# Performance work log

Measured on AMD Instinct MI355X. Metric: run time of the kernel, lower is better.

## Reference

```python
import jax, jax.numpy as jnp
import numpy as np
import math

B, S, D = 2, 2048, 2048
H, KVH, WIN = 16, 4, 256
HD = D // H            # 128
QPER = H // KVH        # 4


def setup_inputs() -> dict:
    key = jax.random.key(0)
    ks = jax.random.split(key, 9)
    s = lambda k, shp: jax.random.normal(k, shp, dtype=jnp.float32) * 0.02
    return {
        "x": jax.random.normal(ks[0], (B, S, D), dtype=jnp.float32),
        "Wq": s(ks[1], (D, D)),            "bq": jnp.zeros((D,), jnp.float32),
        "Wk": s(ks[2], (D, KVH * HD)),      "bk": jnp.zeros((KVH * HD,), jnp.float32),
        "Wv": s(ks[3], (D, KVH * HD)),      "bv": jnp.zeros((KVH * HD,), jnp.float32),
        "Wo": s(ks[4], (D, D)),            "bo": jnp.zeros((D,), jnp.float32),
    }


def reference(x, Wq, bq, Wk, bk, Wv, bv, Wo, bo):
    b, s, _ = x.shape
    # projections
    Q = (x @ Wq + bq).reshape(b, s, H, HD).transpose(0, 2, 1, 3)     # [b,H,s,hd]
    K = (x @ Wk + bk).reshape(b, s, KVH, HD).transpose(0, 2, 1, 3)   # [b,kvh,s,hd]
    V = (x @ Wv + bv).reshape(b, s, KVH, HD).transpose(0, 2, 1, 3)   # [b,kvh,s,hd]
    # GQA grouping: head h = g*QPER + q
    Qg = Q.reshape(b, KVH, QPER, s, HD)                               # [b,g,q,s,hd]
    scores = jnp.einsum('bgqsd,bgtd->bgqst', Qg, K)                   # [b,g,q,s,s]
    i = jnp.arange(s)[:, None]
    j = jnp.arange(s)[None, :]
    keep = (j <= i) & (j >= i - WIN + 1)                              # [s,s]
    scores = jnp.where(keep, scores, -jnp.inf)
    A = jax.nn.softmax(scores / math.sqrt(HD), axis=-1)
    O = jnp.einsum('bgqst,bgtd->bgqsd', A, V)                         # [b,g,q,s,hd]
    O = O.reshape(b, H, s, HD).transpose(0, 2, 1, 3).reshape(b, s, D)
    return O @ Wo + bo
```

## Files before the change

### kernel.cpp

```cpp
#include <hip/hip_runtime.h>
#include <hip/hip_bf16.h>
#include <math.h>

typedef __bf16 bf16_t;
typedef bf16_t bf16x8 __attribute__((ext_vector_type(8)));
typedef bf16_t bf16x4 __attribute__((ext_vector_type(4)));
typedef float  f32x4  __attribute__((ext_vector_type(4)));

#define NB    2
#define SEQ   2048
#define DIM   2048
#define NHEAD 16
#define NKVH  4
#define HDIM  128
#define WINSZ 256
#define KVD   512
#define QKVN  3072
#define MROWS 4096

__device__ __forceinline__ void async_copy16(const void* g, void* lds) {
    __builtin_amdgcn_global_load_lds(
        (const __attribute__((address_space(1))) void*)g,
        (__attribute__((address_space(3))) void*)lds,
        16, 0, 0);
}

__global__ __launch_bounds__(256) void cvt_f32_bf16(const float* __restrict__ in,
                                                    bf16_t* __restrict__ out, int n) {
    int i = (blockIdx.x * 256 + threadIdx.x) * 4;
    if (i >= n) return;
    float4 v = *(const float4*)(in + i);
    bf16x4 o;
    o[0] = (bf16_t)v.x; o[1] = (bf16_t)v.y; o[2] = (bf16_t)v.z; o[3] = (bf16_t)v.w;
    *(bf16x4*)(out + i) = o;
}

__global__ __launch_bounds__(256) void transpose_cvt(const float* __restrict__ in,
                                                     bf16_t* __restrict__ out, int K, int N) {
    __shared__ float tile[32][33];
    int tx = threadIdx.x & 31, ty = threadIdx.x >> 5;
    int n0 = blockIdx.x * 32, k0 = blockIdx.y * 32;
    for (int r = ty; r < 32; r += 8)
        tile[r][tx] = in[(size_t)(k0 + r) * N + n0 + tx];
    __syncthreads();
    for (int r = ty; r < 32; r += 8)
        out[(size_t)(n0 + r) * K + k0 + tx] = (bf16_t)tile[tx][r];
}

__global__ __launch_bounds__(256) void concat_bias(const float* __restrict__ bq,
                                                   const float* __restrict__ bk,
                                                   const float* __restrict__ bv,
                                                   float* __restrict__ out) {
    int i = blockIdx.x * 256 + threadIdx.x;
    if (i >= QKVN) return;
    float v = (i < DIM) ? bq[i] : ((i < DIM + KVD) ? bk[i - DIM] : bv[i - DIM - KVD]);
    out[i] = v;
}

__global__ __launch_bounds__(256) void transpose_v(const bf16_t* __restrict__ QKV,
                                                   bf16_t* __restrict__ Vtb) {
    __shared__ bf16_t t[32][33];
    int tx = threadIdx.x & 31, ty = threadIdx.x >> 5;
    int jb = blockIdx.x, c0 = blockIdx.y * 32, b = blockIdx.z;
    int j0 = jb * 32;
    for (int r = ty; r < 32; r += 8)
        t[r][tx] = QKV[((size_t)(b * SEQ) + j0 + r) * QKVN + (DIM + KVD) + c0 + tx];
    __syncthreads();
    int g = c0 >> 7, dl = c0 & 127;
    bf16_t* outb = Vtb + (((size_t)(b * NKVH) + g) * 64 + jb) * 4096;
    for (int r = ty; r < 32; r += 8)
        outb[(dl + r) * 32 + tx] = t[tx][r];
}

template <int BM, int BN, typename OutT>
__global__ __launch_bounds__(512, 1) void gemm8p(const bf16_t* __restrict__ A,
                                                 const bf16_t* __restrict__ Bt,
                                                 const float* __restrict__ bias,
                                                 OutT* __restrict__ C,
                                                 int M, int N, int K, float qs, int qcols) {
    constexpr int ASLOTS = BM / 16;
    constexpr int BSLOTS = BN / 16;
    constexpr int MF   = BM / 32;
    constexpr int NF   = BN / 64;
    constexpr int AHALF = BM * 32;
    constexpr int BHALF = BN * 32;
    constexpr int BUFSZ = 2 * (AHALF + BHALF);
    __shared__ bf16_t lds[2 * BUFSZ];

    const int tid  = threadIdx.x;
    const int wave = tid >> 6;
    const int lane = tid & 63;
    const int lg = lane >> 4, lc = lane & 15;
    const int wr = wave >> 2, wc = wave & 3;

    const int nbn  = N / BN;
    const int nblk = (M / BM) * nbn;
    const int qq   = nblk >> 3;
    const int swz  = (blockIdx.x & 7) * qq + (blockIdx.x >> 3);
    const long brow = (long)(swz / nbn) * BM;
    const long bcol = (long)(swz % nbn) * BN;

    const int aiss = (ASLOTS - wave + 7) >> 3;
    const int biss = (BSLOTS - wave + 7) >> 3;
    const int miss = aiss + biss;

    f32x4 acc[MF][NF] = {};

    auto stage = [&](int buf, int p, int kt) {
        const int kcol = kt * 64 + p * 32;
        const int srow = lane >> 2;
        const int sch  = lane & 3;
        {
            bf16_t* d = lds + buf * BUFSZ + p * AHALF;
#pragma unroll
            for (int s = wave; s < ASLOTS; s += 8) {
                int row = s * 16 + srow;
                int ch  = sch ^ ((row >> 1) & 3);
                async_copy16(A + (brow + row) * (long)K + kcol + ch * 8, d + s * 512);
            }
        }
        {
            bf16_t* d = lds + buf * BUFSZ + 2 * AHALF + p * BHALF;
#pragma unroll
            for (int s = wave; s < BSLOTS; s += 8) {
                int row = s * 16 + srow;
                int ch  = sch ^ ((row >> 1) & 3);
                async_copy16(Bt + (bcol + row) * (long)K + kcol + ch * 8, d + s * 512);
            }
        }
    };

    stage(0, 0, 0);
    stage(0, 1, 0);

    const int NT = K >> 6;
    const int cswz = (lg ^ ((lc >> 1) & 3)) * 8;
    for (int t = 0; t < NT; ++t) {
#pragma unroll
        for (int p = 0; p < 2; ++p) {
            if (t == NT - 1 && p == 1) {
                asm volatile("s_waitcnt vmcnt(0)" ::: "memory");
            } else if (miss == 4) {
                asm volatile("s_waitcnt vmcnt(4)" ::: "memory");
            } else if (miss == 3) {
                asm volatile("s_waitcnt vmcnt(3)" ::: "memory");
            } else {
                asm volatile("s_waitcnt vmcnt(2)" ::: "memory");
            }
            __builtin_amdgcn_s_barrier();
            asm volatile("" ::: "memory");
            const bf16_t* Ab = lds + (t & 1) * BUFSZ + p * AHALF;
            const bf16_t* Bb = lds + (t & 1) * BUFSZ + 2 * AHALF + p * BHALF;
            bf16x8 af[MF], bv[NF];
#pragma unroll
            for (int m = 0; m < MF; ++m)
                af[m] = *(const bf16x8*)(Ab + (wr * (BM / 2) + m * 16 + lc) * 32 + cswz);
#pragma unroll
            for (int n = 0; n < NF; ++n)
                bv[n] = *(const bf16x8*)(Bb + (wc * (BN / 4) + n * 16 + lc) * 32 + cswz);
            if (t + 1 < NT) stage((t + 1) & 1, p, t + 1);
            __builtin_amdgcn_s_setprio(1);
#pragma unroll
            for (int m = 0; m < MF; ++m)
#pragma unroll
                for (int n = 0; n < NF; ++n)
                    acc[m][n] = __builtin_amdgcn_mfma_f32_16x16x32_bf16(af[m], bv[n], acc[m][n], 0, 0, 0);
            __builtin_amdgcn_s_setprio(0);
        }
    }

#pragma unroll
    for (int n = 0; n < NF; ++n) {
        int gc = (int)bcol + wc * (BN / 4) + n * 16 + lc;
        float bvs = bias[gc];
        bool ds = gc < qcols;
#pragma unroll
        for (int m = 0; m < MF; ++m) {
            long gr = brow + wr * (BM / 2) + m * 16 + 4 * lg;
#pragma unroll
            for (int r = 0; r < 4; ++r) {
                float v = acc[m][n][r] + bvs;
                if (ds) v *= qs;
                C[(gr + r) * (long)N + gc] = (OutT)v;
            }
        }
    }
}

__global__ __launch_bounds__(256) void attn_kernel(const bf16_t* __restrict__ QKV,
                                                   const bf16_t* __restrict__ Vtb,
                                                   bf16_t* __restrict__ Ob) {
    __shared__ bf16_t Kls[2][32 * 128];
    __shared__ bf16_t Vls[2][128 * 32];
    __shared__ bf16_t Pls[4][16 * 40];

    const int wv   = threadIdx.x >> 6;
    const int lane = threadIdx.x & 63;
    const int lg = lane >> 4, lc = lane & 15;

    const int swb = (blockIdx.x & 7) * 128 + (blockIdx.x >> 3);
    const int ti = swb & 127;
    const int g  = (swb >> 7) & 3;
    const int b  = swb >> 9;
    const int h  = g * 4 + wv;
    const int i0 = ti * 16;
    const int irow = i0 + lc;
    bf16_t* P = &Pls[wv][0];

    bf16x8 qf[4];
    {
        const bf16_t* qp = QKV + ((size_t)(b * SEQ) + irow) * QKVN + h * HDIM + lg * 8;
#pragma unroll
        for (int kk = 0; kk < 4; ++kk) qf[kk] = *(const bf16x8*)(qp + kk * 32);
    }

    auto stage = [&](int buf, int jb) {
        const int j0s = jb * 32;
        const bf16_t* kgb = QKV + ((size_t)(b * SEQ) + j0s) * QKVN + DIM + g * HDIM;
#pragma unroll
        for (int ii = 0; ii < 2; ++ii) {
            int i = wv * 2 + ii;
            int row = i * 4 + (lane >> 4);
            int ch  = (lane & 15) ^ (row & 7);
            async_copy16(kgb + (size_t)row * QKVN + ch * 8, &Kls[buf][i * 512]);
        }
        const bf16_t* vgb = Vtb + (((size_t)(b * NKVH) + g) * 64 + jb) * 4096;
#pragma unroll
        for (int ii = 0; ii < 2; ++ii) {
            int i = wv * 2 + ii;
            int row = i * 16 + (lane >> 2);
            int ch  = (lane & 3) ^ ((row ^ (row >> 2)) & 3);
            async_copy16(vgb + row * 32 + ch * 8, &Vls[buf][i * 512]);
        }
    };

    float m_run = -1e30f, l_run = 0.f;
    f32x4 oacc[8] = {};

    int jlo = i0 - (WINSZ - 1); if (jlo < 0) jlo = 0;
    const int jb0 = jlo >> 5;
    const int jb1 = (i0 + 15) >> 5;

    stage(0, jb0);

    for (int jb = jb0; jb <= jb1; ++jb) {
        const int j0 = jb * 32;
        const int cur = (jb - jb0) & 1;
        asm volatile("s_waitcnt vmcnt(0)" ::: "memory");
        __builtin_amdgcn_s_barrier();
        asm volatile("" ::: "memory");

        bf16x8 kf[2][4];
#pragma unroll
        for (int t = 0; t < 2; ++t)
#pragma unroll
            for (int kk = 0; kk < 4; ++kk) {
                int row = t * 16 + lc;
                int ch  = (kk * 4 + lg) ^ (row & 7);
                kf[t][kk] = *(const bf16x8*)(&Kls[cur][row * 128 + ch * 8]);
            }
        if (jb < jb1) stage(cur ^ 1, jb + 1);
        asm volatile("s_waitcnt lgkmcnt(0)" ::: "memory");
        __builtin_amdgcn_sched_barrier(0);

        f32x4 s[2];
        __builtin_amdgcn_s_setprio(1);
#pragma unroll
        for (int t = 0; t < 2; ++t) {
            f32x4 sv = {};
#pragma unroll
            for (int kk = 0; kk < 4; ++kk)
                sv = __builtin_amdgcn_mfma_f32_16x16x32_bf16(kf[t][kk], qf[kk], sv, 0, 0, 0);
            s[t] = sv;
        }
        __builtin_amdgcn_s_setprio(0);

        const bool edge = (j0 < i0 - 240) || (j0 > i0 - 31);
        if (edge) {
#pragma unroll
            for (int t = 0; t < 2; ++t)
#pragma unroll
                for (int r = 0; r < 4; ++r) {
                    int j = j0 + t * 16 + 4 * lg + r;
                    if (j > irow || j < irow - (WINSZ - 1)) s[t][r] = -1e30f;
                }
        }
        float tmax = fmaxf(fmaxf(fmaxf(s[0][0], s[0][1]), fmaxf(s[0][2], s[0][3])),
                           fmaxf(fmaxf(s[1][0], s[1][1]), fmaxf(s[1][2], s[1][3])));
        tmax = fmaxf(tmax, __shfl_xor(tmax, 16, 64));
        tmax = fmaxf(tmax, __shfl_xor(tmax, 32, 64));
        if (!__all(tmax - m_run <= 8.0f)) {
            float m_new = fmaxf(m_run, tmax);
            float resc = __builtin_amdgcn_exp2f(m_run - m_new);
            l_run *= resc;
#pragma unroll
            for (int c = 0; c < 8; ++c) {
                oacc[c][0] *= resc; oacc[c][1] *= resc;
                oacc[c][2] *= resc; oacc[c][3] *= resc;
            }
            m_run = m_new;
        }
        float psum = 0.f;
#pragma unroll
        for (int t = 0; t < 2; ++t) {
            bf16x4 pk;
#pragma unroll
            for (int r = 0; r < 4; ++r) {
                float sv = s[t][r];
                float p = (edge && sv < -5e29f) ? 0.f : __builtin_amdgcn_exp2f(sv - m_run);
                psum += p;
                pk[r] = (bf16_t)p;
            }
            *(bf16x4*)(P + lc * 40 + t * 16 + lg * 4) = pk;
        }
        psum += __shfl_xor(psum, 16, 64);
        psum += __shfl_xor(psum, 32, 64);
        l_run += psum;
        asm volatile("" ::: "memory");

        bf16x8 vf[8];
#pragma unroll
        for (int c = 0; c < 8; ++c) {
            int row = c * 16 + lc;
            int ch  = lg ^ ((row ^ (row >> 2)) & 3);
            vf[c] = *(const bf16x8*)(&Vls[cur][row * 32 + ch * 8]);
        }
        bf16x8 pf = *(const bf16x8*)(P + lc * 40 + lg * 8);

        __builtin_amdgcn_s_setprio(1);
#pragma unroll
        for (int c = 0; c < 8; ++c)
            oacc[c] = __builtin_amdgcn_mfma_f32_16x16x32_bf16(vf[c], pf, oacc[c], 0, 0, 0);
        __builtin_amdgcn_s_setprio(0);
    }

    const float inv = 1.f / l_run;
#pragma unroll
    for (int c = 0; c < 8; ++c) {
        bf16x4 ov;
#pragma unroll
        for (int r = 0; r < 4; ++r) ov[r] = (bf16_t)(oacc[c][r] * inv);
        *(bf16x4*)(Ob + ((size_t)(b * SEQ) + irow) * DIM + h * HDIM + c * 16 + lg * 4) = ov;
    }
}

extern "C" void kernel_launch(void* const* d_in, const int* in_sizes, int n_in,
                              void* d_out, int out_size, void* d_ws, size_t ws_size,
                              hipStream_t stream) {
    const float* x  = (const float*)d_in[0];
    const float* Wq = (const float*)d_in[1];
    const float* bq = (const float*)d_in[2];
    const float* Wk = (const float*)d_in[3];
    const float* bk = (const float*)d_in[4];
    const float* Wv = (const float*)d_in[5];
    const float* bv = (const float*)d_in[6];
    const float* Wo = (const float*)d_in[7];
    const float* bo = (const float*)d_in[8];
    float* out = (float*)d_out;

    char* ws = (char*)d_ws;
    bf16_t* xb    = (bf16_t*)(ws);
    bf16_t* WqkvT = (bf16_t*)(ws + (16u << 20));
    bf16_t* WoT   = (bf16_t*)(ws + (28u << 20));
    bf16_t* QKVb  = (bf16_t*)(ws + (36u << 20));
    float*  bqkv  = (float*) (ws + (60u << 20));
    bf16_t* Vtb   = WqkvT;
    bf16_t* Ob    = xb;

    const float qs = 0.12751707498038074f;

    cvt_f32_bf16<<<(MROWS * DIM) / 1024, 256, 0, stream>>>(x, xb, MROWS * DIM);
    transpose_cvt<<<dim3(DIM / 32, DIM / 32), 256, 0, stream>>>(Wq, WqkvT, DIM, DIM);
    transpose_cvt<<<dim3(KVD / 32, DIM / 32), 256, 0, stream>>>(Wk, WqkvT + (size_t)DIM * DIM, DIM, KVD);
    transpose_cvt<<<dim3(KVD / 32, DIM / 32), 256, 0, stream>>>(Wv, WqkvT + (size_t)(DIM + KVD) * DIM, DIM, KVD);
    transpose_cvt<<<dim3(DIM / 32, DIM / 32), 256, 0, stream>>>(Wo, WoT, DIM, DIM);
    concat_bias<<<(QKVN + 255) / 256, 256, 0, stream>>>(bq, bk, bv, bqkv);

    gemm8p<256, 192, bf16_t><<<dim3((MROWS / 256) * (QKVN / 192)), 512, 0, stream>>>(
        xb, WqkvT, bqkv, QKVb, MROWS, QKVN, DIM, qs, DIM);

    transpose_v<<<dim3(SEQ / 32, KVD / 32, NB), 256, 0, stream>>>(QKVb, Vtb);

    attn_kernel<<<dim3(NB * NKVH * (SEQ / 16)), 256, 0, stream>>>(QKVb, Vtb, Ob);

    gemm8p<128, 256, float><<<dim3((MROWS / 128) * (DIM / 256)), 512, 0, stream>>>(
        Ob, WoT, bo, out, MROWS, DIM, DIM, 1.0f, 0);
}
```

Baseline: 160.8 us.

## Process 32 query rows per attention wave and fuse preprocessing kernels

The attention kernel now handles two 16-row query subtiles per wave, so each staged K/V block in LDS feeds twice as many MFMAs. This halves the grid and cuts redundant K/V loads, at the cost of more registers and fewer blocks for occupancy. The six preprocessing launches (x conversion, four weight transposes, bias concat) are merged into one kernel that dispatches on block index, removing per-launch overhead.

Measured after the change: 147.6 us. 1.09x faster.

```diff
diff --git a/kernel.cpp b/kernel.cpp
--- a/kernel.cpp
+++ b/kernel.cpp
@@ -25,36 +25,47 @@
         16, 0, 0);
 }
 
-__global__ __launch_bounds__(256) void cvt_f32_bf16(const float* __restrict__ in,
-                                                    bf16_t* __restrict__ out, int n) {
-    int i = (blockIdx.x * 256 + threadIdx.x) * 4;
-    if (i >= n) return;
-    float4 v = *(const float4*)(in + i);
-    bf16x4 o;
-    o[0] = (bf16_t)v.x; o[1] = (bf16_t)v.y; o[2] = (bf16_t)v.z; o[3] = (bf16_t)v.w;
-    *(bf16x4*)(out + i) = o;
-}
-
-__global__ __launch_bounds__(256) void transpose_cvt(const float* __restrict__ in,
-                                                     bf16_t* __restrict__ out, int K, int N) {
+__global__ __launch_bounds__(256) void preprocess(
+    const float* __restrict__ x,  const float* __restrict__ Wq,
+    const float* __restrict__ bq, const float* __restrict__ Wk,
+    const float* __restrict__ bk, const float* __restrict__ Wv,
+    const float* __restrict__ bv, const float* __restrict__ Wo,
+    bf16_t* __restrict__ xb, bf16_t* __restrict__ WqkvT,
+    bf16_t* __restrict__ WoT, float* __restrict__ bqkv) {
     __shared__ float tile[32][33];
-    int tx = threadIdx.x & 31, ty = threadIdx.x >> 5;
-    int n0 = blockIdx.x * 32, k0 = blockIdx.y * 32;
+    const int tid = threadIdx.x;
+    int bid = blockIdx.x;
+    if (bid < 8192) {
+        int i = (bid * 256 + tid) * 4;
+        float4 v = *(const float4*)(x + i);
+        bf16x4 o;
+        o[0] = (bf16_t)v.x; o[1] = (bf16_t)v.y; o[2] = (bf16_t)v.z; o[3] = (bf16_t)v.w;
+        *(bf16x4*)(xb + i) = o;
+        return;
+    }
+    bid -= 8192;
+    const float* src; bf16_t* dst; int N;
+    if (bid < 4096)       { src = Wq; dst = WqkvT;                          N = DIM; }
+    else if (bid < 5120)  { src = Wk; dst = WqkvT + (size_t)DIM * DIM;      N = KVD; bid -= 4096; }
+    else if (bid < 6144)  { src = Wv; dst = WqkvT + (size_t)(DIM+KVD)*DIM;  N = KVD; bid -= 5120; }
+    else if (bid < 10240) { src = Wo; dst = WoT;                            N = DIM; bid -= 6144; }
+    else {
+        int i = (bid - 10240) * 256 + tid;
+        if (i < QKVN) {
+            float v = (i < DIM) ? bq[i] : ((i < DIM + KVD) ? bk[i - DIM] : bv[i - DIM - KVD]);
+            bqkv[i] = v;
+        }
+        return;
+    }
+    const int K = DIM;
+    int ntile = N / 32;
+    int n0 = (bid % ntile) * 32, k0 = (bid / ntile) * 32;
+    int tx = tid & 31, ty = tid >> 5;
     for (int r = ty; r < 32; r += 8)
-        tile[r][tx] = in[(size_t)(k0 + r) * N + n0 + tx];
+        tile[r][tx] = src[(size_t)(k0 + r) * N + n0 + tx];
     __syncthreads();
     for (int r = ty; r < 32; r += 8)
-        out[(size_t)(n0 + r) * K + k0 + tx] = (bf16_t)tile[tx][r];
-}
-
-__global__ __launch_bounds__(256) void concat_bias(const float* __restrict__ bq,
-                                                   const float* __restrict__ bk,
-                                                   const float* __restrict__ bv,
-                                                   float* __restrict__ out) {
-    int i = blockIdx.x * 256 + threadIdx.x;
-    if (i >= QKVN) return;
-    float v = (i < DIM) ? bq[i] : ((i < DIM + KVD) ? bk[i - DIM] : bv[i - DIM - KVD]);
-    out[i] = v;
+        dst[(size_t)(n0 + r) * K + k0 + tx] = (bf16_t)tile[tx][r];
 }
 
 __global__ __launch_bounds__(256) void transpose_v(const bf16_t* __restrict__ QKV,
@@ -192,26 +203,26 @@
                                                    bf16_t* __restrict__ Ob) {
     __shared__ bf16_t Kls[2][32 * 128];
     __shared__ bf16_t Vls[2][128 * 32];
-    __shared__ bf16_t Pls[4][16 * 40];
+    __shared__ bf16_t Pls[4][32 * 40];
 
     const int wv   = threadIdx.x >> 6;
     const int lane = threadIdx.x & 63;
     const int lg = lane >> 4, lc = lane & 15;
 
-    const int swb = (blockIdx.x & 7) * 128 + (blockIdx.x >> 3);
-    const int ti = swb & 127;
-    const int g  = (swb >> 7) & 3;
-    const int b  = swb >> 9;
+    const int swb = (blockIdx.x & 7) * 64 + (blockIdx.x >> 3);
+    const int ti = swb & 63;
+    const int g  = (swb >> 6) & 3;
+    const int b  = swb >> 8;
     const int h  = g * 4 + wv;
-    const int i0 = ti * 16;
-    const int irow = i0 + lc;
+    const int i0 = ti * 32;
     bf16_t* P = &Pls[wv][0];
 
-    bf16x8 qf[4];
-    {
-        const bf16_t* qp = QKV + ((size_t)(b * SEQ) + irow) * QKVN + h * HDIM + lg * 8;
-#pragma unroll
-        for (int kk = 0; kk < 4; ++kk) qf[kk] = *(const bf16x8*)(qp + kk * 32);
+    bf16x8 qf[2][4];
+#pragma unroll
+    for (int sq = 0; sq < 2; ++sq) {
+        const bf16_t* qp = QKV + ((size_t)(b * SEQ) + i0 + sq * 16 + lc) * QKVN + h * HDIM + lg * 8;
+#pragma unroll
+        for (int kk = 0; kk < 4; ++kk) qf[sq][kk] = *(const bf16x8*)(qp + kk * 32);
     }
 
     auto stage = [&](int buf, int jb) {
@@ -234,12 +245,12 @@
         }
     };
 
-    float m_run = -1e30f, l_run = 0.f;
-    f32x4 oacc[8] = {};
+    float m_run[2] = {-1e30f, -1e30f}, l_run[2] = {0.f, 0.f};
+    f32x4 oacc[2][8] = {};
 
     int jlo = i0 - (WINSZ - 1); if (jlo < 0) jlo = 0;
     const int jb0 = jlo >> 5;
-    const int jb1 = (i0 + 15) >> 5;
+    const int jb1 = (i0 + 31) >> 5;
 
     stage(0, jb0);
 
@@ -263,59 +274,79 @@
         asm volatile("s_waitcnt lgkmcnt(0)" ::: "memory");
         __builtin_amdgcn_sched_barrier(0);
 
-        f32x4 s[2];
+        f32x4 s[2][2];
         __builtin_amdgcn_s_setprio(1);
 #pragma unroll
-        for (int t = 0; t < 2; ++t) {
-            f32x4 sv = {};
-#pragma unroll
-            for (int kk = 0; kk < 4; ++kk)
-                sv = __builtin_amdgcn_mfma_f32_16x16x32_bf16(kf[t][kk], qf[kk], sv, 0, 0, 0);
-            s[t] = sv;
-        }
+        for (int t = 0; t < 2; ++t)
+#pragma unroll
+            for (int sq = 0; sq < 2; ++sq) {
+                f32x4 sv = {};
+#pragma unroll
+                for (int kk = 0; kk < 4; ++kk)
+                    sv = __builtin_amdgcn_mfma_f32_16x16x32_bf16(kf[t][kk], qf[sq][kk], sv, 0, 0, 0);
+                s[t][sq] = sv;
+            }
         __builtin_amdgcn_s_setprio(0);
 
-        const bool edge = (j0 < i0 - 240) || (j0 > i0 - 31);
+        const bool edge = (j0 < i0 - (WINSZ - 32)) || (j0 > i0 - 31);
         if (edge) {
 #pragma unroll
             for (int t = 0; t < 2; ++t)
 #pragma unroll
+                for (int sq = 0; sq < 2; ++sq) {
+                    int irow = i0 + sq * 16 + lc;
+#pragma unroll
+                    for (int r = 0; r < 4; ++r) {
+                        int j = j0 + t * 16 + 4 * lg + r;
+                        if (j > irow || j < irow - (WINSZ - 1)) s[t][sq][r] = -1e30f;
+                    }
+                }
+        }
+        float tmax[2];
+#pragma unroll
+        for (int sq = 0; sq < 2; ++sq) {
+            float tm = fmaxf(fmaxf(fmaxf(s[0][sq][0], s[0][sq][1]), fmaxf(s[0][sq][2], s[0][sq][3])),
+                             fmaxf(fmaxf(s[1][sq][0], s[1][sq][1]), fmaxf(s[1][sq][2], s[1][sq][3])));
+            tm = fmaxf(tm, __shfl_xor(tm, 16, 64));
+            tm = fmaxf(tm, __shfl_xor(tm, 32, 64));
+            tmax[sq] = tm;
+        }
+        if (!__all(tmax[0] - m_run[0] <= 8.0f && tmax[1] - m_run[1] <= 8.0f)) {
+#pragma unroll
+            for (int sq = 0; sq < 2; ++sq) {
+                float m_new = fmaxf(m_run[sq], tmax[sq]);
+                float resc = __builtin_amdgcn_exp2f(m_run[sq] - m_new);
+                l_run[sq] *= resc;
+#pragma unroll
+                for (int c = 0; c < 8; ++c) {
+                    oacc[sq][c][0] *= resc; oacc[sq][c][1] *= resc;
+                    oacc[sq][c][2] *= resc; oacc[sq][c][3] *= resc;
+                }
+                m_run[sq] = m_new;
+            }
+        }
+        float psum[2] = {0.f, 0.f};
+#pragma unroll
+        for (int t = 0; t < 2; ++t)
+#pragma unroll
+            for (int sq = 0; sq < 2; ++sq) {
+                bf16x4 pk;
+#pragma unroll
                 for (int r = 0; r < 4; ++r) {
-                    int j = j0 + t * 16 + 4 * lg + r;
-                    if (j > irow || j < irow - (WINSZ - 1)) s[t][r] = -1e30f;
+                    float sv = s[t][sq][r];
+                    float p = (edge && sv < -5e29f) ? 0.f : __builtin_amdgcn_exp2f(sv - m_run[sq]);
+                    psum[sq] += p;
+                    pk[r] = (bf16_t)p;
                 }
-        }
-        float tmax = fmaxf(fmaxf(fmaxf(s[0][0], s[0][1]), fmaxf(s[0][2], s[0][3])),
-                           fmaxf(fmaxf(s[1][0], s[1][1]), fmaxf(s[1][2], s[1][3])));
-        tmax = fmaxf(tmax, __shfl_xor(tmax, 16, 64));
-        tmax = fmaxf(tmax, __shfl_xor(tmax, 32, 64));
-        if (!__all(tmax - m_run <= 8.0f)) {
-            float m_new = fmaxf(m_run, tmax);
-            float resc = __builtin_amdgcn_exp2f(m_run - m_new);
-            l_run *= resc;
-#pragma unroll
-            for (int c = 0; c < 8; ++c) {
-                oacc[c][0] *= resc; oacc[c][1] *= resc;
-                oacc[c][2] *= resc; oacc[c][3] *= resc;
-            }
-            m_run = m_new;
-        }
-        float psum = 0.f;
-#pragma unroll
-        for (int t = 0; t < 2; ++t) {
-            bf16x4 pk;
-#pragma unroll
-            for (int r = 0; r < 4; ++r) {
-                float sv = s[t][r];
-                float p = (edge && sv < -5e29f) ? 0.f : __builtin_amdgcn_exp2f(sv - m_run);
-                psum += p;
-                pk[r] = (bf16_t)p;
-            }
-            *(bf16x4*)(P + lc * 40 + t * 16 + lg * 4) = pk;
-        }
-        psum += __shfl_xor(psum, 16, 64);
-        psum += __shfl_xor(psum, 32, 64);
-        l_run += psum;
+                *(bf16x4*)(P + (sq * 16 + lc) * 40 + t * 16 + lg * 4) = pk;
+            }
+#pragma unroll
+        for (int sq = 0; sq < 2; ++sq) {
+            float ps = psum[sq];
+            ps += __shfl_xor(ps, 16, 64);
+            ps += __shfl_xor(ps, 32, 64);
+            l_run[sq] += ps;
+        }
         asm volatile("" ::: "memory");
 
         bf16x8 vf[8];
@@ -325,22 +356,30 @@
             int ch  = lg ^ ((row ^ (row >> 2)) & 3);
             vf[c] = *(const bf16x8*)(&Vls[cur][row * 32 + ch * 8]);
         }
-        bf16x8 pf = *(const bf16x8*)(P + lc * 40 + lg * 8);
+        bf16x8 pf[2];
+#pragma unroll
+        for (int sq = 0; sq < 2; ++sq)
+            pf[sq] = *(const bf16x8*)(P + (sq * 16 + lc) * 40 + lg * 8);
 
         __builtin_amdgcn_s_setprio(1);
 #pragma unroll
         for (int c = 0; c < 8; ++c)
-            oacc[c] = __builtin_amdgcn_mfma_f32_16x16x32_bf16(vf[c], pf, oacc[c], 0, 0, 0);
+#pragma unroll
+            for (int sq = 0; sq < 2; ++sq)
+                oacc[sq][c] = __builtin_amdgcn_mfma_f32_16x16x32_bf16(vf[c], pf[sq], oacc[sq][c], 0, 0, 0);
         __builtin_amdgcn_s_setprio(0);
     }
 
-    const float inv = 1.f / l_run;
-#pragma unroll
-    for (int c = 0; c < 8; ++c) {
-        bf16x4 ov;
-#pragma unroll
-        for (int r = 0; r < 4; ++r) ov[r] = (bf16_t)(oacc[c][r] * inv);
-        *(bf16x4*)(Ob + ((size_t)(b * SEQ) + irow) * DIM + h * HDIM + c * 16 + lg * 4) = ov;
+#pragma unroll
+    for (int sq = 0; sq < 2; ++sq) {
+        const float inv = 1.f / l_run[sq];
+#pragma unroll
+        for (int c = 0; c < 8; ++c) {
+            bf16x4 ov;
+#pragma unroll
+            for (int r = 0; r < 4; ++r) ov[r] = (bf16_t)(oacc[sq][c][r] * inv);
+            *(bf16x4*)(Ob + ((size_t)(b * SEQ) + i0 + sq * 16 + lc) * DIM + h * HDIM + c * 16 + lg * 4) = ov;
+        }
     }
 }
 
@@ -369,19 +408,15 @@
 
     const float qs = 0.12751707498038074f;
 
-    cvt_f32_bf16<<<(MROWS * DIM) / 1024, 256, 0, stream>>>(x, xb, MROWS * DIM);
-    transpose_cvt<<<dim3(DIM / 32, DIM / 32), 256, 0, stream>>>(Wq, WqkvT, DIM, DIM);
-    transpose_cvt<<<dim3(KVD / 32, DIM / 32), 256, 0, stream>>>(Wk, WqkvT + (size_t)DIM * DIM, DIM, KVD);
-    transpose_cvt<<<dim3(KVD / 32, DIM / 32), 256, 0, stream>>>(Wv, WqkvT + (size_t)(DIM + KVD) * DIM, DIM, KVD);
-    transpose_cvt<<<dim3(DIM / 32, DIM / 32), 256, 0, stream>>>(Wo, WoT, DIM, DIM);
-    concat_bias<<<(QKVN + 255) / 256, 256, 0, stream>>>(bq, bk, bv, bqkv);
+    preprocess<<<18444, 256, 0, stream>>>(x, Wq, bq, Wk, bk, Wv, bv, Wo,
+                                          xb, WqkvT, WoT, bqkv);
 
     gemm8p<256, 192, bf16_t><<<dim3((MROWS / 256) * (QKVN / 192)), 512, 0, stream>>>(
         xb, WqkvT, bqkv, QKVb, MROWS, QKVN, DIM, qs, DIM);
 
     transpose_v<<<dim3(SEQ / 32, KVD / 32, NB), 256, 0, stream>>>(QKVb, Vtb);
 
-    attn_kernel<<<dim3(NB * NKVH * (SEQ / 16)), 256, 0, stream>>>(QKVb, Vtb, Ob);
+    attn_kernel<<<dim3(NB * NKVH * (SEQ / 32)), 256, 0, stream>>>(QKVb, Vtb, Ob);
 
     gemm8p<128, 256, float><<<dim3((MROWS / 128) * (DIM / 256)), 512, 0, stream>>>(
         Ob, WoT, bo, out, MROWS, DIM, DIM, 1.0f, 0);
```
